# Optimization experiments

Measured on AMD Instinct MI355X. Metric: run time of the kernel, lower is better.

## Reference

```python
import jax, jax.numpy as jnp
import numpy as np

B = 16          # number of trees (batch)
H = 256         # hidden_size == feature_size
S = 16          # Tree.num_sem
C = 5           # max_child_num (complete C-ary tree)
L = 6           # tree depth: leaves at level L, internal levels 0..L-1
N_LEAF = C**L                     # 15625
N_INT = (C**L - 1) // (C - 1)     # 3906 internal nodes, level-l offset = (C^l-1)/(C-1)


def setup_inputs() -> dict:
    key = jax.random.key(0)
    ks = jax.random.split(key, 20)
    rn = lambda k, shp, s=0.05: jax.random.normal(k, shp, dtype=jnp.float32) * s
    return {
        "leaf_box": jax.random.normal(ks[0], (B, N_LEAF, 4), dtype=jnp.float32),
        "leaf_sem": jax.random.uniform(ks[1], (B, N_LEAF, S), dtype=jnp.float32),
        "internal_box": jax.random.normal(ks[2], (B, N_INT, 4), dtype=jnp.float32),
        "node_type": jax.random.randint(ks[3], (B, N_INT), 0, 3, dtype=jnp.int32),
        "eps": jax.random.normal(ks[4], (B, H), dtype=jnp.float32),
        "W_box": rn(ks[5], (4, H)), "b_box": jnp.zeros((H,), jnp.float32),
        "W_sem": rn(ks[6], (S, H)), "b_sem": jnp.zeros((H,), jnp.float32),
        "W_node": rn(ks[7], (3, C * H, H)), "b_node": jnp.zeros((3, H), jnp.float32),
        "W1": rn(ks[8], (H, H)), "b1": jnp.zeros((H,), jnp.float32),
        "Wmu": rn(ks[9], (H, H)), "bmu": jnp.zeros((H,), jnp.float32),
        "Wvar": rn(ks[10], (H, H)), "bvar": jnp.zeros((H,), jnp.float32),
    }


def reference(leaf_box, leaf_sem, internal_box, node_type, eps,
              W_box, b_box, W_sem, b_sem, W_node, b_node,
              W1, b1, Wmu, bmu, Wvar, bvar):
    box_enc = lambda b: jax.nn.relu(b @ W_box + b_box)
    # LeafEncoder: relu-box-encoding + relu-sem-encoding
    feats = box_enc(leaf_box) + jax.nn.relu(leaf_sem @ W_sem + b_sem)  # [B, N_LEAF, H]
    # Bottom-up over internal levels (static loop over L=6 levels)
    for l in range(L - 1, -1, -1):
        n = C ** l
        off = (C ** l - 1) // (C - 1)
        child = feats.reshape(B, n, C * H)  # children flattened per parent (child_exists==1)
        # Apply all 3 branch encoders (vertical/horizontal/stack), select by node label
        y_all = jnp.einsum('bnk,tkh->bnth', child, W_node) + b_node          # [B,n,3,H]
        sel = jax.nn.one_hot(node_type[:, off:off + n], 3, dtype=child.dtype)  # [B,n,3]
        y = jnp.einsum('bnth,bnt->bnh', y_all, sel)
        feats = jax.nn.relu(y) + box_enc(internal_box[:, off:off + n])
    root = feats[:, 0]  # [B, H]
    # Sampler (variational, probabilistic)
    enc = jax.nn.relu(root @ W1 + b1)
    mu = enc @ Wmu + bmu
    logvar = enc @ Wvar + bvar
    std = jnp.exp(0.5 * logvar)
    kld = 1.0 + logvar - mu ** 2 - jnp.exp(logvar)
    return jnp.concatenate([eps * std + mu, kld], axis=1)  # [B, 2H]
```

## Files before the change

### kernel.cpp

```cpp
#include <hip/hip_runtime.h>


#define B_ 16
#define H_ 256
#define NLEAF 15625
#define NINT 3906
#define RND128(x) (((x) + 127) & ~127)

typedef __bf16 bf16_t;
typedef bf16_t bf16x8 __attribute__((ext_vector_type(8)));
typedef bf16_t bf16x4 __attribute__((ext_vector_type(4)));
typedef float f32x4 __attribute__((ext_vector_type(4)));

__device__ __forceinline__ void gl2lds16(const bf16_t* g, bf16_t* l) {
  __builtin_amdgcn_global_load_lds((const __attribute__((address_space(1))) void*)g,
                                   (__attribute__((address_space(3))) void*)l,
                                   16, 0, 0);
}

__global__ __launch_bounds__(256) void prep_kernel(const float* __restrict__ W_node,
                                                   bf16_t* __restrict__ Wt,
                                                   int* __restrict__ counters) {
  if (blockIdx.x == 0 && threadIdx.x < 18) counters[threadIdx.x] = 0;
  const int t = blockIdx.x / 80;
  const int kc = blockIdx.x % 80;
  const int h = threadIdx.x;
  const int half = h >> 7, r = h & 127;
  const int sw = (r >> 1) & 3;
  const float* srcp = W_node + (size_t)t * 1280 * 256 + h;
  bf16_t* base = Wt + ((size_t)(t * 2 + half) * 40) * 4096 + r * 32;
#pragma unroll
  for (int k0 = kc * 16; k0 < kc * 16 + 16; k0 += 8) {
    bf16x8 v;
#pragma unroll
    for (int j = 0; j < 8; ++j) v[j] = (bf16_t)srcp[(size_t)(k0 + j) * 256];
    const int ks = k0 >> 5;
    const int q = (k0 >> 3) & 3;
    *(bf16x8*)(base + (size_t)ks * 4096 + ((q ^ sw) << 3)) = v;
  }
}

__global__ __launch_bounds__(256) void bucket_kernel(const int* __restrict__ node_type,
                                                     int* __restrict__ counters,
                                                     int2* __restrict__ buckets) {
  __shared__ int lcnt[18];
  __shared__ int lbase[18];
  const int tid = threadIdx.x;
  if (tid < 18) lcnt[tid] = 0;
  __syncthreads();

  int idx = blockIdx.x * 256 + tid;
  bool active = idx < B_ * NINT;
  int t = 0, key = 0, mypos = 0;
  int2 e;
  int base = 0, nl_cap = 0;
  if (active) {
    int b = idx / NINT;
    int j = idx - b * NINT;
    int l, off;
    if (j >= 781)      { l = 5; off = 781; }
    else if (j >= 156) { l = 4; off = 156; }
    else if (j >= 31)  { l = 3; off = 31; }
    else if (j >= 6)   { l = 2; off = 6; }
    else if (j >= 1)   { l = 1; off = 1; }
    else               { l = 0; off = 0; }
    const int n_tab[6]    = {1, 5, 25, 125, 625, 3125};
    const int nn_tab[6]   = {5, 25, 125, 625, 3125, 15625};
    const int base_tab[6] = {0, 48, 288, 1488, 7488, 37488};
    int n_l = n_tab[l], nn = nn_tab[l];
    t = node_type[idx];
    int i = j - off;
    e.x = b * n_l + i;
    e.y = b * nn + 5 * i;
    base = base_tab[l];
    nl_cap = B_ * n_l;
    key = l * 3 + t;
    mypos = atomicAdd(&lcnt[key], 1);
  }
  __syncthreads();
  if (tid < 18) {
    int c = lcnt[tid];
    lbase[tid] = c ? atomicAdd(&counters[tid], c) : 0;
  }
  __syncthreads();
  if (active) {
    buckets[base + t * nl_cap + lbase[key] + mypos] = e;
  }
}

__global__ __launch_bounds__(256) void dest_kernel(const int2* __restrict__ buckets,
                                                   const int* __restrict__ counters,
                                                   int* __restrict__ wdest_all,
                                                   int* __restrict__ rsrc6) {
  int flat = blockIdx.x * 256 + threadIdx.x;
  if (flat >= 187488) return;
  int l, base, cap, coff;
  if (flat >= 37488)      { l = 5; base = 37488; cap = 50000; coff = 0; }
  else if (flat >= 7488)  { l = 4; base = 7488;  cap = 10000; coff = 12480; }
  else if (flat >= 1488)  { l = 3; base = 1488;  cap = 2000;  coff = 2480; }
  else if (flat >= 288)   { l = 2; base = 288;   cap = 400;   coff = 480; }
  else if (flat >= 48)    { l = 1; base = 48;    cap = 80;    coff = 80; }
  else                    { l = 0; base = 0;     cap = 16;    coff = 0; }
  int rel = flat - base;
  int t = (rel >= 2 * cap) ? 2 : (rel >= cap ? 1 : 0);
  int s = rel - t * cap;
  const int* c3 = counters + l * 3;
  if (s >= c3[t]) return;
  int pfxr = (t > 0 ? RND128(c3[0]) : 0) + (t > 1 ? RND128(c3[1]) : 0);
  int R = pfxr + s;
  int2 e = buckets[flat];
  if (l == 5) {
    int* rp = rsrc6 + 5 * R;
#pragma unroll
    for (int c = 0; c < 5; ++c) rp[c] = e.y + c;
  } else {
    int* wp = wdest_all + coff + 5 * e.x;
#pragma unroll
    for (int c = 0; c < 5; ++c) wp[c] = (R << 3) + c;
  }
}

__global__ __launch_bounds__(256) void leaf_kernel(
    const float* __restrict__ leaf_box, const float* __restrict__ leaf_sem,
    const float* __restrict__ W_box, const float* __restrict__ b_box,
    const float* __restrict__ W_sem, const float* __restrict__ b_sem,
    const int* __restrict__ rsrc, bf16_t* __restrict__ g5) {
  const int lane = threadIdx.x & 63;
  const int wave = threadIdx.x >> 6;
  const int q = lane >> 4;
  const int c = lane & 15;
  const int hh = wave & 1;
  const int gw = wave >> 1;

  bf16x8 wsem[8], wbox[8];
#pragma unroll
  for (int T = 0; T < 8; ++T) {
    const int hb = (hh * 8 + T) * 16 + c;
    bf16x8 a;
#pragma unroll
    for (int j = 0; j < 8; ++j) a[j] = (bf16_t)0.f;
    if (q < 2) {
#pragma unroll
      for (int j = 0; j < 8; ++j) a[j] = (bf16_t)W_sem[(q * 8 + j) * H_ + hb];
    } else if (q == 2) {
      a[0] = (bf16_t)b_sem[hb];
    }
    wsem[T] = a;
    bf16x8 b;
#pragma unroll
    for (int j = 0; j < 8; ++j) b[j] = (bf16_t)0.f;
    if (q == 0) {
#pragma unroll
      for (int j = 0; j < 4; ++j) b[j] = (bf16_t)W_box[j * H_ + hb];
      b[4] = (bf16_t)b_box[hb];
    }
    wbox[T] = b;
  }

  const int NG2 = 15705;
  const int gstride = gridDim.x * 2;
  for (int g = blockIdx.x * 2 + gw; g < NG2; g += gstride) {
    const int ci = g * 16 + c;
    int row = rsrc[ci];
    row = ((unsigned)row < (unsigned)(B_ * NLEAF)) ? row : 0;
    const int R = ci / 5;
    const int c5 = ci - R * 5;
    bf16x8 xs, xb;
#pragma unroll
    for (int j = 0; j < 8; ++j) { xs[j] = (bf16_t)0.f; xb[j] = (bf16_t)0.f; }
    if (q < 2) {
      const float4* sp = (const float4*)(leaf_sem + (size_t)row * 16 + q * 8);
      float4 s0 = sp[0], s1 = sp[1];
      xs[0] = (bf16_t)s0.x; xs[1] = (bf16_t)s0.y; xs[2] = (bf16_t)s0.z; xs[3] = (bf16_t)s0.w;
      xs[4] = (bf16_t)s1.x; xs[5] = (bf16_t)s1.y; xs[6] = (bf16_t)s1.z; xs[7] = (bf16_t)s1.w;
    } else if (q == 2) {
      xs[0] = (bf16_t)1.0f;
    }
    if (q == 0) {
      float4 bx = *(const float4*)(leaf_box + (size_t)row * 4);
      xb[0] = (bf16_t)bx.x; xb[1] = (bf16_t)bx.y; xb[2] = (bf16_t)bx.z; xb[3] = (bf16_t)bx.w;
      xb[4] = (bf16_t)1.0f;
    }
    const int rr = R & 127;
    const int sw = (rr >> 1) & 3;
    bf16_t* obase = g5 + (size_t)(R >> 7) * 163840 + rr * 32;
#pragma unroll
    for (int T = 0; T < 8; ++T) {
      f32x4 z = {0.f, 0.f, 0.f, 0.f};
      f32x4 as = __builtin_amdgcn_mfma_f32_16x16x32_bf16(wsem[T], xs, z, 0, 0, 0);
      f32x4 ab = __builtin_amdgcn_mfma_f32_16x16x32_bf16(wbox[T], xb, z, 0, 0, 0);
      bf16x4 o;
#pragma unroll
      for (int r = 0; r < 4; ++r)
        o[r] = (bf16_t)(fmaxf(as[r], 0.f) + fmaxf(ab[r], 0.f));
      const int ks = c5 * 8 + hh * 4 + (T >> 1);
      const int pc = (((T & 1) << 1) | (q >> 1)) ^ sw;
      *(bf16x4*)(obase + (size_t)ks * 4096 + (pc << 3) + ((q & 1) << 2)) = o;
    }
  }
}

__device__ __forceinline__ void level_phase(
    int x, const bf16_t* __restrict__ src, bf16_t* __restrict__ dst,
    const int2* __restrict__ bucket, const int* __restrict__ counters,
    const bf16_t* __restrict__ Wt, const float* __restrict__ b_node,
    const float* __restrict__ ibox, const float* __restrict__ W_box,
    const float* __restrict__ b_box, const int* __restrict__ wdest,
    int n_l, int off_l, int cap, int P,
    bf16_t Asm[3][128][32], bf16_t Bsm[3][128][32]) {
  if (x >= 6 * P) return;
  const int t = x / (2 * P);
  const int r2 = x - t * 2 * P;
  const int nblk = r2 / P;
  const int p = r2 - nblk * P;
  const int cnt = counters[t];
  const int tile0 = p * 128;
  if (tile0 >= cnt) return;
  const int pfxr = (t > 0 ? RND128(counters[0]) : 0) + (t > 1 ? RND128(counters[1]) : 0);
  const int2* rd = bucket + (size_t)t * cap;

  const int tid = threadIdx.x;
  const int lane = tid & 63;
  const int wave = tid >> 6;
  const int wm = wave & 1, wn = wave >> 1;
  const int quad = lane >> 4;
  const int l15 = lane & 15;

  const bf16_t* ga0 = src + (size_t)(pfxr + tile0) * 1280 + wave * 1024 + (lane << 3);
  const bf16_t* gb0 = Wt + ((size_t)(t * 2 + nblk) * 40) * 4096 + wave * 1024 + (lane << 3);

  f32x4 acc[4][4];
#pragma unroll
  for (int i = 0; i < 4; ++i)
#pragma unroll
    for (int j = 0; j < 4; ++j) acc[i][j] = (f32x4){0.f, 0.f, 0.f, 0.f};

  const int pcs = (quad ^ ((l15 >> 1) & 3)) * 8;

#define STG2(buf, ks)                                   \
  {                                                     \
    const bf16_t* ga = ga0 + (ks) * 4096;               \
    const bf16_t* gb = gb0 + (ks) * 4096;               \
    bf16_t* la = &Asm[buf][0][0] + wave * 1024;         \
    bf16_t* lb = &Bsm[buf][0][0] + wave * 1024;         \
    gl2lds16(ga, la);                                   \
    gl2lds16(ga + 512, la + 512);                       \
    gl2lds16(gb, lb);                                   \
    gl2lds16(gb + 512, lb + 512);                       \
  }
#define FRG2(bufv)                                                            \
  {                                                                           \
    bf16x8 af[4], bfr[4];                                                     \
    _Pragma("unroll") for (int am = 0; am < 4; ++am)                          \
        af[am] = *(const bf16x8*)(&Asm[bufv][wm * 64 + am * 16 + l15][pcs]);  \
    _Pragma("unroll") for (int bn = 0; bn < 4; ++bn)                          \
        bfr[bn] = *(const bf16x8*)(&Bsm[bufv][wn * 64 + bn * 16 + l15][pcs]); \
    __builtin_amdgcn_s_setprio(1);                                            \
    _Pragma("unroll") for (int am = 0; am < 4; ++am)                          \
        _Pragma("unroll") for (int bn = 0; bn < 4; ++bn)                      \
            acc[am][bn] = __builtin_amdgcn_mfma_f32_16x16x32_bf16(            \
                af[am], bfr[bn], acc[am][bn], 0, 0, 0);                       \
    __builtin_amdgcn_s_setprio(0);                                            \
  }

  STG2(0, 0)
  STG2(1, 1)
  int rbuf = 0, wbuf = 2;
  for (int ks = 0; ks < 38; ++ks) {
    asm volatile("s_waitcnt vmcnt(4)" ::: "memory");
    __builtin_amdgcn_s_barrier();
    {
      bf16x8 af[4], bfr[4];
#pragma unroll
      for (int am = 0; am < 4; ++am)
        af[am] = *(const bf16x8*)(&Asm[rbuf][wm * 64 + am * 16 + l15][pcs]);
#pragma unroll
      for (int bn = 0; bn < 4; ++bn)
        bfr[bn] = *(const bf16x8*)(&Bsm[rbuf][wn * 64 + bn * 16 + l15][pcs]);
      STG2(wbuf, ks + 2)
      __builtin_amdgcn_s_setprio(1);
#pragma unroll
      for (int am = 0; am < 4; ++am)
#pragma unroll
        for (int bn = 0; bn < 4; ++bn)
          acc[am][bn] = __builtin_amdgcn_mfma_f32_16x16x32_bf16(af[am], bfr[bn], acc[am][bn], 0, 0, 0);
      __builtin_amdgcn_s_setprio(0);
    }
    rbuf = (rbuf + 1 == 3) ? 0 : rbuf + 1;
    wbuf = (wbuf + 1 == 3) ? 0 : wbuf + 1;
  }
  asm volatile("s_waitcnt vmcnt(4)" ::: "memory");
  __builtin_amdgcn_s_barrier();
  FRG2(rbuf)
  rbuf = (rbuf + 1 == 3) ? 0 : rbuf + 1;
  asm volatile("s_waitcnt vmcnt(0)" ::: "memory");
  __builtin_amdgcn_s_barrier();
  FRG2(rbuf)
#undef FRG2
#undef STG2

  float wbv[4][6];
#pragma unroll
  for (int bn = 0; bn < 4; ++bn) {
    int col = nblk * 128 + wn * 64 + bn * 16 + l15;
    wbv[bn][0] = W_box[col];
    wbv[bn][1] = W_box[H_ + col];
    wbv[bn][2] = W_box[2 * H_ + col];
    wbv[bn][3] = W_box[3 * H_ + col];
    wbv[bn][4] = b_box[col];
    wbv[bn][5] = b_node[t * H_ + col];
  }
#pragma unroll
  for (int am = 0; am < 4; ++am) {
    int orw_[4]; float4 bxv[4]; bool valid[4];
#pragma unroll
    for (int r = 0; r < 4; ++r) {
      int gidx = tile0 + wm * 64 + am * 16 + quad * 4 + r;
      valid[r] = (gidx < cnt);
      int ic = valid[r] ? gidx : (cnt - 1);
      int orw = rd[ic].x;
      orw_[r] = orw;
      int b = orw / n_l;
      int i = orw - b * n_l;
      bxv[r] = *(const float4*)(ibox + ((size_t)b * NINT + off_l + i) * 4);
    }
    if (wdest) {
      size_t ob[4]; int sw_[4];
#pragma unroll
      for (int r = 0; r < 4; ++r) {
        int wd = wdest[orw_[r]];
        int R = wd >> 3, cc = wd & 7;
        int rr = R & 127;
        ob[r] = (size_t)(R >> 7) * 163840 + (size_t)cc * 32768 + (size_t)rr * 32;
        sw_[r] = (rr >> 1) & 3;
      }
#pragma unroll
      for (int bn = 0; bn < 4; ++bn) {
        int col = nblk * 128 + wn * 64 + bn * 16 + l15;
        int kc2 = col >> 5, qq = (col >> 3) & 3, ww = col & 7;
#pragma unroll
        for (int r = 0; r < 4; ++r) {
          if (!valid[r]) continue;
          float y = fmaxf(acc[am][bn][r] + wbv[bn][5], 0.f);
          float be = fmaf(wbv[bn][0], bxv[r].x,
                     fmaf(wbv[bn][1], bxv[r].y,
                     fmaf(wbv[bn][2], bxv[r].z,
                     fmaf(wbv[bn][3], bxv[r].w, wbv[bn][4]))));
          be = fmaxf(be, 0.f);
          dst[ob[r] + (size_t)kc2 * 4096 + ((qq ^ sw_[r]) << 3) + ww] = (bf16_t)(y + be);
        }
      }
    } else {
#pragma unroll
      for (int bn = 0; bn < 4; ++bn) {
        int col = nblk * 128 + wn * 64 + bn * 16 + l15;
#pragma unroll
        for (int r = 0; r < 4; ++r) {
          if (!valid[r]) continue;
          float y = fmaxf(acc[am][bn][r] + wbv[bn][5], 0.f);
          float be = fmaf(wbv[bn][0], bxv[r].x,
                     fmaf(wbv[bn][1], bxv[r].y,
                     fmaf(wbv[bn][2], bxv[r].z,
                     fmaf(wbv[bn][3], bxv[r].w, wbv[bn][4]))));
          be = fmaxf(be, 0.f);
          dst[(size_t)orw_[r] * H_ + col] = (bf16_t)(y + be);
        }
      }
    }
  }
}

__global__ __launch_bounds__(256) void level5_kernel(
    const bf16_t* __restrict__ src, bf16_t* __restrict__ dst,
    const int2* __restrict__ bucket, const int* __restrict__ counters,
    const bf16_t* __restrict__ Wt, const float* __restrict__ b_node,
    const float* __restrict__ ibox, const float* __restrict__ W_box,
    const float* __restrict__ b_box, const int* __restrict__ wdest,
    int n_l, int off_l, int cap) {
  __shared__ __align__(16) bf16_t Asm[3][128][32];
  __shared__ __align__(16) bf16_t Bsm[3][128][32];
  const int x = blockIdx.x;
  const int p = ((x >> 4) << 3) + (x & 7);
  const int nblk = (x >> 3) & 1;
  const int t = blockIdx.y;
  const int P = gridDim.x / 2;
  const int xx = t * 2 * P + nblk * P + p;
  level_phase(xx, src, dst, bucket, counters, Wt, b_node, ibox, W_box, b_box,
              wdest, n_l, off_l, cap, P, Asm, Bsm);
}

__global__ __launch_bounds__(256, 2) void level_direct(
    const bf16_t* __restrict__ src, bf16_t* __restrict__ dst,
    const int2* __restrict__ bucket, const int* __restrict__ counters,
    const bf16_t* __restrict__ Wt, const float* __restrict__ b_node,
    const float* __restrict__ ibox, const float* __restrict__ W_box,
    const float* __restrict__ b_box, const int* __restrict__ wdest,
    int n_l, int off_l, int cap, int TP) {
  const int sl = blockIdx.x;
  const int t = sl / TP;
  const int s = sl - t * TP;
  const int cnt = counters[t];
  const int tile0 = s * 16;
  if (tile0 >= cnt) return;
  const int pfxr = (t > 0 ? RND128(counters[0]) : 0) + (t > 1 ? RND128(counters[1]) : 0);
  const int2* rd = bucket + (size_t)t * cap;

  const int tid = threadIdx.x;
  const int lane = tid & 63;
  const int wave = tid >> 6;
  const int quad = lane >> 4;
  const int l15 = lane & 15;
  const int pcs = (quad ^ ((l15 >> 1) & 3)) * 8;

  const int Rbase = pfxr + tile0;
  const bf16_t* aptr = src + (size_t)(Rbase >> 7) * 163840 +
                       ((Rbase & 127) + l15) * 32 + pcs;
  const bf16_t* bptr[4];
  int cols[4];
#pragma unroll
  for (int bn = 0; bn < 4; ++bn) {
    int col = wave * 64 + bn * 16 + l15;
    cols[bn] = col;
    bptr[bn] = Wt + (size_t)(t * 2 + (col >> 7)) * 163840 + (col & 127) * 32 + pcs;
  }

  f32x4 acc[4];
#pragma unroll
  for (int bn = 0; bn < 4; ++bn) acc[bn] = (f32x4){0.f, 0.f, 0.f, 0.f};
#pragma unroll
  for (int g = 0; g < 10; ++g) {
    bf16x8 af[4], b0[4], b1[4], b2[4], b3[4];
#pragma unroll
    for (int i = 0; i < 4; ++i) {
      const size_t o = (size_t)(g * 4 + i) * 4096;
      af[i] = *(const bf16x8*)(aptr + o);
      b0[i] = *(const bf16x8*)(bptr[0] + o);
      b1[i] = *(const bf16x8*)(bptr[1] + o);
      b2[i] = *(const bf16x8*)(bptr[2] + o);
      b3[i] = *(const bf16x8*)(bptr[3] + o);
    }
#pragma unroll
    for (int i = 0; i < 4; ++i) {
      acc[0] = __builtin_amdgcn_mfma_f32_16x16x32_bf16(af[i], b0[i], acc[0], 0, 0, 0);
      acc[1] = __builtin_amdgcn_mfma_f32_16x16x32_bf16(af[i], b1[i], acc[1], 0, 0, 0);
      acc[2] = __builtin_amdgcn_mfma_f32_16x16x32_bf16(af[i], b2[i], acc[2], 0, 0, 0);
      acc[3] = __builtin_amdgcn_mfma_f32_16x16x32_bf16(af[i], b3[i], acc[3], 0, 0, 0);
    }
  }

  int orw_[4]; float4 bxv[4]; bool valid[4];
#pragma unroll
  for (int r = 0; r < 4; ++r) {
    int gidx = tile0 + quad * 4 + r;
    valid[r] = (gidx < cnt);
    int ic = valid[r] ? gidx : (cnt - 1);
    int orw = rd[ic].x;
    orw_[r] = orw;
    int b = orw / n_l;
    int i = orw - b * n_l;
    bxv[r] = *(const float4*)(ibox + ((size_t)b * NINT + off_l + i) * 4);
  }
  if (wdest) {
    size_t ob[4]; int swz[4];
#pragma unroll
    for (int r = 0; r < 4; ++r) {
      int wd = wdest[orw_[r]];
      int R = wd >> 3, cc = wd & 7;
      int rr = R & 127;
      ob[r] = (size_t)(R >> 7) * 163840 + (size_t)cc * 32768 + (size_t)rr * 32;
      swz[r] = (rr >> 1) & 3;
    }
#pragma unroll
    for (int bn = 0; bn < 4; ++bn) {
      int col = cols[bn];
      float w0 = W_box[col], w1 = W_box[H_ + col], w2 = W_box[2 * H_ + col];
      float w3 = W_box[3 * H_ + col], w4 = b_box[col];
      float bn5 = b_node[t * H_ + col];
      int kc2 = col >> 5, qq = (col >> 3) & 3, ww = col & 7;
#pragma unroll
      for (int r = 0; r < 4; ++r) {
        if (!valid[r]) continue;
        float y = fmaxf(acc[bn][r] + bn5, 0.f);
        float be = fmaf(w0, bxv[r].x, fmaf(w1, bxv[r].y,
                   fmaf(w2, bxv[r].z, fmaf(w3, bxv[r].w, w4))));
        be = fmaxf(be, 0.f);
        dst[ob[r] + (size_t)kc2 * 4096 + ((size_t)(qq ^ swz[r]) << 3) + ww] =
            (bf16_t)(y + be);
      }
    }
  } else {
#pragma unroll
    for (int bn = 0; bn < 4; ++bn) {
      int col = cols[bn];
      float w0 = W_box[col], w1 = W_box[H_ + col], w2 = W_box[2 * H_ + col];
      float w3 = W_box[3 * H_ + col], w4 = b_box[col];
      float bn5 = b_node[t * H_ + col];
#pragma unroll
      for (int r = 0; r < 4; ++r) {
        if (!valid[r]) continue;
        float y = fmaxf(acc[bn][r] + bn5, 0.f);
        float be = fmaf(w0, bxv[r].x, fmaf(w1, bxv[r].y,
                   fmaf(w2, bxv[r].z, fmaf(w3, bxv[r].w, w4))));
        be = fmaxf(be, 0.f);
        dst[(size_t)orw_[r] * H_ + col] = (bf16_t)(y + be);
      }
    }
  }
}

__global__ __launch_bounds__(256) void head_kernel(
    const bf16_t* __restrict__ f0, const float* __restrict__ eps,
    const float* __restrict__ W1, const float* __restrict__ b1,
    const float* __restrict__ Wmu, const float* __restrict__ bmu,
    const float* __restrict__ Wvar, const float* __restrict__ bvar,
    float* __restrict__ out) {
  __shared__ float root[256];
  __shared__ float enc[256];
  int b = blockIdx.x, h = threadIdx.x;
  root[h] = (float)f0[b * H_ + h];
  __syncthreads();
  float a = b1[h];
  for (int k = 0; k < 256; ++k) a = fmaf(root[k], W1[k * H_ + h], a);
  enc[h] = fmaxf(a, 0.f);
  __syncthreads();
  float m = bmu[h], lv = bvar[h];
  for (int k = 0; k < 256; ++k) {
    float e = enc[k];
    m = fmaf(e, Wmu[k * H_ + h], m);
    lv = fmaf(e, Wvar[k * H_ + h], lv);
  }
  float stdv = expf(0.5f * lv);
  float kld = 1.f + lv - m * m - expf(lv);
  out[b * 512 + h] = eps[b * H_ + h] * stdv + m;
  out[b * 512 + 256 + h] = kld;
}

extern "C" void kernel_launch(void* const* d_in, const int* in_sizes, int n_in,
                              void* d_out, int out_size, void* d_ws, size_t ws_size,
                              hipStream_t stream) {
  const float* leaf_box     = (const float*)d_in[0];
  const float* leaf_sem     = (const float*)d_in[1];
  const float* internal_box = (const float*)d_in[2];
  const int*   node_type    = (const int*)d_in[3];
  const float* eps          = (const float*)d_in[4];
  const float* W_box        = (const float*)d_in[5];
  const float* b_box        = (const float*)d_in[6];
  const float* W_sem        = (const float*)d_in[7];
  const float* b_sem        = (const float*)d_in[8];
  const float* W_node       = (const float*)d_in[9];
  const float* b_node       = (const float*)d_in[10];
  const float* W1           = (const float*)d_in[11];
  const float* b1           = (const float*)d_in[12];
  const float* Wmu          = (const float*)d_in[13];
  const float* bmu          = (const float*)d_in[14];
  const float* Wvar         = (const float*)d_in[15];
  const float* bvar         = (const float*)d_in[16];
  float* out = (float*)d_out;

  char* p = (char*)d_ws;
  auto alloc = [&](size_t bytes) {
    char* r = p;
    p += (bytes + 255) & ~(size_t)255;
    return r;
  };
  const int n_tab[6] = {1, 5, 25, 125, 625, 3125};
  bf16_t* Wt = (bf16_t*)alloc((size_t)3 * 2 * 40 * 4096 * 2);
  bf16_t* f0 = (bf16_t*)alloc((size_t)B_ * H_ * 2);
  bf16_t* G[6];
  for (int l = 0; l <= 5; ++l)
    G[l] = (bf16_t*)alloc(((size_t)B_ * n_tab[l] + 384) * 1280 * 2);
  int* counters  = (int*)alloc(128 * 4);
  int2* buckets  = (int2*)alloc((size_t)187488 * 8);
  int* wdest_all = (int*)alloc((size_t)62480 * 4);
  int* rsrc6     = (int*)alloc((size_t)251280 * 4);

  hipLaunchKernelGGL(prep_kernel, dim3(240), dim3(256), 0, stream, W_node, Wt, counters);
  hipLaunchKernelGGL(bucket_kernel, dim3((B_ * NINT + 255) / 256), dim3(256), 0, stream,
                     node_type, counters, buckets);
  hipLaunchKernelGGL(dest_kernel, dim3((187488 + 255) / 256), dim3(256), 0, stream,
                     buckets, counters, wdest_all, rsrc6);
  hipLaunchKernelGGL(leaf_kernel, dim3(1024), dim3(256), 0, stream,
                     leaf_box, leaf_sem, W_box, b_box, W_sem, b_sem, rsrc6, G[5]);

  {
    int cap = B_ * n_tab[5];
    int tiles = (cap + 127) / 128;
    int tiles8 = (tiles + 7) & ~7;
    hipLaunchKernelGGL(level5_kernel, dim3(2 * tiles8, 3), dim3(256), 0, stream,
                       G[5], G[4], buckets + 37488, counters + 15,
                       Wt, b_node, internal_box, W_box, b_box,
                       wdest_all + 12480, 3125, 781, cap);
  }

  const int lvl_base[6] = {0, 48, 288, 1488, 7488, 37488};
  const int off_tab[6]  = {0, 1, 6, 31, 156, 781};
  const int woff[6]     = {0, 0, 80, 480, 2480, 12480};
  for (int l = 4; l >= 0; --l) {
    int TP = n_tab[l];
    const int* wdp = (l >= 1) ? (wdest_all + woff[l]) : nullptr;
    bf16_t* dstp = (l >= 1) ? G[l - 1] : f0;
    hipLaunchKernelGGL(level_direct, dim3(3 * TP), dim3(256), 0, stream,
                       G[l], dstp, buckets + lvl_base[l], counters + l * 3,
                       Wt, b_node, internal_box, W_box, b_box, wdp,
                       n_tab[l], off_tab[l], B_ * n_tab[l], TP);
  }
  hipLaunchKernelGGL(head_kernel, dim3(16), dim3(256), 0, stream,
                     f0, eps, W1, b1, Wmu, bmu, Wvar, bvar, out);
}
```

Measured before the change: 349.0 us.

## Load level-5 weight fragments directly to registers, dropping B-tile LDS staging

The level-5 GEMM kernel stops staging the weight (B) tile through shared memory. Each wave now loads its bf16 weight fragments straight from global memory into registers, double-buffered across k-steps, while the activation tile keeps its three-stage LDS pipeline. This halves LDS use and sets launch bounds to 4 blocks per CU to raise occupancy, but each wave now fetches its weights separately and register pressure goes up. The unused non-wdest store path is also removed.

```diff
diff --git a/kernel.cpp b/kernel.cpp
--- a/kernel.cpp
+++ b/kernel.cpp
@@ -200,19 +200,18 @@
   }
 }
 
-__device__ __forceinline__ void level_phase(
-    int x, const bf16_t* __restrict__ src, bf16_t* __restrict__ dst,
+__global__ __launch_bounds__(256, 4) void level5_kernel(
+    const bf16_t* __restrict__ src, bf16_t* __restrict__ dst,
     const int2* __restrict__ bucket, const int* __restrict__ counters,
     const bf16_t* __restrict__ Wt, const float* __restrict__ b_node,
     const float* __restrict__ ibox, const float* __restrict__ W_box,
     const float* __restrict__ b_box, const int* __restrict__ wdest,
-    int n_l, int off_l, int cap, int P,
-    bf16_t Asm[3][128][32], bf16_t Bsm[3][128][32]) {
-  if (x >= 6 * P) return;
-  const int t = x / (2 * P);
-  const int r2 = x - t * 2 * P;
-  const int nblk = r2 / P;
-  const int p = r2 - nblk * P;
+    int n_l, int off_l, int cap) {
+  __shared__ __align__(16) bf16_t Asm[3][128][32];
+  const int x = blockIdx.x;
+  const int p = ((x >> 4) << 3) + (x & 7);
+  const int nblk = (x >> 3) & 1;
+  const int t = blockIdx.y;
   const int cnt = counters[t];
   const int tile0 = p * 128;
   if (tile0 >= cnt) return;
@@ -225,9 +224,15 @@
   const int wm = wave & 1, wn = wave >> 1;
   const int quad = lane >> 4;
   const int l15 = lane & 15;
+  const int pcs = (quad ^ ((l15 >> 1) & 3)) * 8;
 
   const bf16_t* ga0 = src + (size_t)(pfxr + tile0) * 1280 + wave * 1024 + (lane << 3);
-  const bf16_t* gb0 = Wt + ((size_t)(t * 2 + nblk) * 40) * 4096 + wave * 1024 + (lane << 3);
+  const bf16_t* gb[4];
+#pragma unroll
+  for (int bn = 0; bn < 4; ++bn) {
+    int colh = wn * 64 + bn * 16 + l15;
+    gb[bn] = Wt + (size_t)(t * 2 + nblk) * 163840 + (size_t)colh * 32 + pcs;
+  }
 
   f32x4 acc[4][4];
 #pragma unroll
@@ -235,69 +240,51 @@
 #pragma unroll
     for (int j = 0; j < 4; ++j) acc[i][j] = (f32x4){0.f, 0.f, 0.f, 0.f};
 
-  const int pcs = (quad ^ ((l15 >> 1) & 3)) * 8;
-
-#define STG2(buf, ks)                                   \
+#define STG5(buf, ks)                                   \
   {                                                     \
     const bf16_t* ga = ga0 + (ks) * 4096;               \
-    const bf16_t* gb = gb0 + (ks) * 4096;               \
     bf16_t* la = &Asm[buf][0][0] + wave * 1024;         \
-    bf16_t* lb = &Bsm[buf][0][0] + wave * 1024;         \
     gl2lds16(ga, la);                                   \
     gl2lds16(ga + 512, la + 512);                       \
-    gl2lds16(gb, lb);                                   \
-    gl2lds16(gb + 512, lb + 512);                       \
-  }
-#define FRG2(bufv)                                                            \
+  }
+
+  bf16x8 bb0[4], bb1[4];
+  STG5(0, 0)
+#pragma unroll
+  for (int bn = 0; bn < 4; ++bn) bb0[bn] = *(const bf16x8*)(gb[bn]);
+  STG5(1, 1)
+
+  int rbuf = 0, wbuf = 2;
+#define BODY5(ks, BCUR, BNXT)                                                 \
   {                                                                           \
-    bf16x8 af[4], bfr[4];                                                     \
+    if ((ks) == 39) asm volatile("s_waitcnt vmcnt(0)" ::: "memory");          \
+    else            asm volatile("s_waitcnt vmcnt(2)" ::: "memory");          \
+    __builtin_amdgcn_s_barrier();                                             \
+    bf16x8 af[4];                                                             \
     _Pragma("unroll") for (int am = 0; am < 4; ++am)                          \
-        af[am] = *(const bf16x8*)(&Asm[bufv][wm * 64 + am * 16 + l15][pcs]);  \
-    _Pragma("unroll") for (int bn = 0; bn < 4; ++bn)                          \
-        bfr[bn] = *(const bf16x8*)(&Bsm[bufv][wn * 64 + bn * 16 + l15][pcs]); \
+      af[am] = *(const bf16x8*)(&Asm[rbuf][wm * 64 + am * 16 + l15][pcs]);    \
+    if ((ks) + 1 < 40) {                                                      \
+      _Pragma("unroll") for (int bn = 0; bn < 4; ++bn)                        \
+        BNXT[bn] = *(const bf16x8*)(gb[bn] + ((ks) + 1) * 4096);              \
+    }                                                                         \
+    if ((ks) + 2 < 40) STG5(wbuf, (ks) + 2)                                   \
     __builtin_amdgcn_s_setprio(1);                                            \
     _Pragma("unroll") for (int am = 0; am < 4; ++am)                          \
-        _Pragma("unroll") for (int bn = 0; bn < 4; ++bn)                      \
-            acc[am][bn] = __builtin_amdgcn_mfma_f32_16x16x32_bf16(            \
-                af[am], bfr[bn], acc[am][bn], 0, 0, 0);                       \
+      _Pragma("unroll") for (int bn = 0; bn < 4; ++bn)                        \
+        acc[am][bn] = __builtin_amdgcn_mfma_f32_16x16x32_bf16(                \
+            af[am], BCUR[bn], acc[am][bn], 0, 0, 0);                          \
     __builtin_amdgcn_s_setprio(0);                                            \
-  }
-
-  STG2(0, 0)
-  STG2(1, 1)
-  int rbuf = 0, wbuf = 2;
-  for (int ks = 0; ks < 38; ++ks) {
-    asm volatile("s_waitcnt vmcnt(4)" ::: "memory");
-    __builtin_amdgcn_s_barrier();
-    {
-      bf16x8 af[4], bfr[4];
-#pragma unroll
-      for (int am = 0; am < 4; ++am)
-        af[am] = *(const bf16x8*)(&Asm[rbuf][wm * 64 + am * 16 + l15][pcs]);
-#pragma unroll
-      for (int bn = 0; bn < 4; ++bn)
-        bfr[bn] = *(const bf16x8*)(&Bsm[rbuf][wn * 64 + bn * 16 + l15][pcs]);
-      STG2(wbuf, ks + 2)
-      __builtin_amdgcn_s_setprio(1);
-#pragma unroll
-      for (int am = 0; am < 4; ++am)
-#pragma unroll
-        for (int bn = 0; bn < 4; ++bn)
-          acc[am][bn] = __builtin_amdgcn_mfma_f32_16x16x32_bf16(af[am], bfr[bn], acc[am][bn], 0, 0, 0);
-      __builtin_amdgcn_s_setprio(0);
-    }
-    rbuf = (rbuf + 1 == 3) ? 0 : rbuf + 1;
-    wbuf = (wbuf + 1 == 3) ? 0 : wbuf + 1;
-  }
-  asm volatile("s_waitcnt vmcnt(4)" ::: "memory");
-  __builtin_amdgcn_s_barrier();
-  FRG2(rbuf)
-  rbuf = (rbuf + 1 == 3) ? 0 : rbuf + 1;
-  asm volatile("s_waitcnt vmcnt(0)" ::: "memory");
-  __builtin_amdgcn_s_barrier();
-  FRG2(rbuf)
-#undef FRG2
-#undef STG2
+    rbuf = (rbuf + 1 == 3) ? 0 : rbuf + 1;                                    \
+    wbuf = (wbuf + 1 == 3) ? 0 : wbuf + 1;                                    \
+  }
+
+  for (int kk = 0; kk < 20; ++kk) {
+    const int ks = kk * 2;
+    BODY5(ks, bb0, bb1)
+    BODY5(ks + 1, bb1, bb0)
+  }
+#undef BODY5
+#undef STG5
 
   float wbv[4][6];
 #pragma unroll
@@ -324,7 +311,7 @@
       int i = orw - b * n_l;
       bxv[r] = *(const float4*)(ibox + ((size_t)b * NINT + off_l + i) * 4);
     }
-    if (wdest) {
+    {
       size_t ob[4]; int sw_[4];
 #pragma unroll
       for (int r = 0; r < 4; ++r) {
@@ -350,43 +337,8 @@
           dst[ob[r] + (size_t)kc2 * 4096 + ((qq ^ sw_[r]) << 3) + ww] = (bf16_t)(y + be);
         }
       }
-    } else {
-#pragma unroll
-      for (int bn = 0; bn < 4; ++bn) {
-        int col = nblk * 128 + wn * 64 + bn * 16 + l15;
-#pragma unroll
-        for (int r = 0; r < 4; ++r) {
-          if (!valid[r]) continue;
-          float y = fmaxf(acc[am][bn][r] + wbv[bn][5], 0.f);
-          float be = fmaf(wbv[bn][0], bxv[r].x,
-                     fmaf(wbv[bn][1], bxv[r].y,
-                     fmaf(wbv[bn][2], bxv[r].z,
-                     fmaf(wbv[bn][3], bxv[r].w, wbv[bn][4]))));
-          be = fmaxf(be, 0.f);
-          dst[(size_t)orw_[r] * H_ + col] = (bf16_t)(y + be);
-        }
-      }
-    }
-  }
-}
-
-__global__ __launch_bounds__(256) void level5_kernel(
-    const bf16_t* __restrict__ src, bf16_t* __restrict__ dst,
-    const int2* __restrict__ bucket, const int* __restrict__ counters,
-    const bf16_t* __restrict__ Wt, const float* __restrict__ b_node,
-    const float* __restrict__ ibox, const float* __restrict__ W_box,
-    const float* __restrict__ b_box, const int* __restrict__ wdest,
-    int n_l, int off_l, int cap) {
-  __shared__ __align__(16) bf16_t Asm[3][128][32];
-  __shared__ __align__(16) bf16_t Bsm[3][128][32];
-  const int x = blockIdx.x;
-  const int p = ((x >> 4) << 3) + (x & 7);
-  const int nblk = (x >> 3) & 1;
-  const int t = blockIdx.y;
-  const int P = gridDim.x / 2;
-  const int xx = t * 2 * P + nblk * P + p;
-  level_phase(xx, src, dst, bucket, counters, Wt, b_node, ibox, W_box, b_box,
-              wdest, n_l, off_l, cap, P, Asm, Bsm);
+    }
+  }
 }
 
 __global__ __launch_bounds__(256, 2) void level_direct(
```

Result: slower. 375.8 us (+7.7%).
